# Optimization experiments

Hardware: AMD Instinct MI355X
Metric: run time of the kernel (lower is better)

Reference implementation:

```python
import jax, jax.numpy as jnp
import numpy as np

NEG_SLOPE = 0.2

def gat_conv(x, src, dst, W, a_src, a_dst, b, num_nodes, concat):
    # PyG GATConv (add_self_loops already applied to src/dst).
    H, C = a_src.shape
    h = (x @ W).reshape(-1, H, C)                      # [N,H,C]
    s = jnp.einsum('nhc,hc->nh', h, a_src)             # per-node src score
    d = jnp.einsum('nhc,hc->nh', h, a_dst)             # per-node dst score
    e = jax.nn.leaky_relu(s[src] + d[dst], NEG_SLOPE)  # [E,H]
    emax = jax.lax.stop_gradient(
        jax.ops.segment_max(e, dst, num_segments=num_nodes))  # [N,H]
    ex = jnp.exp(e - emax[dst])
    denom = jax.ops.segment_sum(ex, dst, num_segments=num_nodes)
    alpha = ex / denom[dst]                            # segment softmax over in-edges
    msg = h[src] * alpha[:, :, None]                   # [E,H,C]
    out = jax.ops.segment_sum(msg, dst, num_segments=num_nodes)
    out = out.reshape(num_nodes, H * C) if concat else out.mean(axis=1)
    return out + b

def setup_inputs() -> dict:
    key = jax.random.key(0)
    ks = jax.random.split(key, 20)
    N, E, F = 50000, 400000, 256
    x = jax.random.normal(ks[0], (N, F), dtype=jnp.float32)
    edge_index = jax.random.randint(ks[1], (2, E), 0, N, dtype=jnp.int64)
    def p(k, shape):
        return (jax.random.normal(k, shape, dtype=jnp.float32) * 0.1)
    inp = {'x': x, 'edge_index': edge_index}
    # conv1: 256 -> 8x32 ; conv2: 256 -> 4x32 ; conv3: 128 -> 2x32 ; conv4: 64 -> 1x32
    dims = [(256, 8, 32), (256, 4, 32), (128, 2, 32), (64, 1, 32)]
    ki = 2
    for i, (fin, H, C) in enumerate(dims, start=1):
        inp[f'W{i}'] = p(ks[ki], (fin, H * C)); ki += 1
        inp[f'a_src{i}'] = p(ks[ki], (H, C)); ki += 1
        inp[f'a_dst{i}'] = p(ks[ki], (H, C)); ki += 1
        bdim = H * C if i < 4 else C
        inp[f'b{i}'] = jnp.zeros((bdim,), dtype=jnp.float32)
    return inp

def reference(x, edge_index, W1, a_src1, a_dst1, b1, W2, a_src2, a_dst2, b2,
              W3, a_src3, a_dst3, b3, W4, a_src4, a_dst4, b4):
    N = x.shape[0]
    loops = jnp.arange(N, dtype=edge_index.dtype)
    src = jnp.concatenate([edge_index[0], loops])
    dst = jnp.concatenate([edge_index[1], loops])
    h = jax.nn.elu(gat_conv(x, src, dst, W1, a_src1, a_dst1, b1, N, True))
    h = jax.nn.elu(gat_conv(h, src, dst, W2, a_src2, a_dst2, b2, N, True))
    h = gat_conv(h, src, dst, W3, a_src3, a_dst3, b3, N, True)
    h = jax.nn.elu(h)
    h = gat_conv(h, src, dst, W4, a_src4, a_dst4, b4, N, False)
    return jax.nn.log_softmax(h, axis=1)
```

## Files before the change

kernel.cpp:

```cpp
#include <hip/hip_runtime.h>
#include <hip/hip_bf16.h>

#define LRELU_SLOPE 0.2f

typedef __attribute__((ext_vector_type(8))) short short8;
typedef __attribute__((ext_vector_type(4))) float f32x4;

__device__ __forceinline__ unsigned short bf16r(float f) {
    unsigned int u = __builtin_bit_cast(unsigned int, f);
    u += 0x7fffu + ((u >> 16) & 1u);
    return (unsigned short)(u >> 16);
}
__device__ __forceinline__ float bf2f(unsigned short u) {
    return __builtin_bit_cast(float, (unsigned int)u << 16);
}


#define WTOT 108544

__global__ void k_pre(const float* __restrict__ Wa, const float* __restrict__ Wb,
                      const float* __restrict__ Wc, const float* __restrict__ Wd,
                      unsigned short* __restrict__ Ta, unsigned short* __restrict__ Tb,
                      unsigned short* __restrict__ Tc, unsigned short* __restrict__ Td,
                      const int* __restrict__ ei, int* __restrict__ cnt, int E, int N) {
    int gid = blockIdx.x * blockDim.x + threadIdx.x;
    if (gid < WTOT) {
        int id = gid;
        const float* W; unsigned short* T; int K, Nc;
        if (id < 65536)       { W = Wa; T = Ta; K = 256; Nc = 256; }
        else if (id < 98304)  { id -= 65536;  W = Wb; T = Tb; K = 256; Nc = 128; }
        else if (id < 106496) { id -= 98304;  W = Wc; T = Tc; K = 128; Nc = 64; }
        else                  { id -= 106496; W = Wd; T = Td; K = 64;  Nc = 32; }
        int n = id / K, k = id % K;
        T[id] = bf16r(W[(long)k * Nc + n]);
        return;
    }
    int e = gid - WTOT;
    if (e >= E + N) return;
    int dst = (e < E) ? ei[E + e] : (e - E);
    atomicAdd(&cnt[dst], 1);
}


__global__ void k_scan_blk(const int* __restrict__ cnt, int* __restrict__ offs,
                           int* __restrict__ bsum, int N) {
    __shared__ int temp[1024];
    int t = threadIdx.x;
    int gi = blockIdx.x * 1024 + t;
    int v = (gi < N) ? cnt[gi] : 0;
    temp[t] = v;
    __syncthreads();
    for (int o = 1; o < 1024; o <<= 1) {
        int x = (t >= o) ? temp[t - o] : 0;
        __syncthreads();
        temp[t] += x;
        __syncthreads();
    }
    if (gi < N) offs[gi] = temp[t] - v;
    if (t == 1023) bsum[blockIdx.x] = temp[1023];
}

__global__ void k_scan(const int* __restrict__ cnt, int* __restrict__ offs, int N) {
    __shared__ int temp[1024];
    __shared__ int carry_s;
    int t = threadIdx.x;
    if (t == 0) carry_s = 0;
    __syncthreads();
    for (int base = 0; base < N; base += 1024) {
        int v = (base + t < N) ? cnt[base + t] : 0;
        temp[t] = v;
        __syncthreads();
        for (int o = 1; o < 1024; o <<= 1) {
            int x = (t >= o) ? temp[t - o] : 0;
            __syncthreads();
            temp[t] += x;
            __syncthreads();
        }
        int incl = temp[t];
        int carry = carry_s;
        if (base + t < N) offs[base + t] = carry + incl - v;
        __syncthreads();
        if (t == 1023) carry_s = carry + temp[1023];
        __syncthreads();
    }
    if (t == 0) offs[N] = carry_s;
}

__global__ void k_scan_add(int* __restrict__ offs, const int* __restrict__ bpre,
                           int* __restrict__ wp, int N, int nb) {
    int gi = blockIdx.x * blockDim.x + threadIdx.x;
    if (gi < N) {
        int v = offs[gi] + bpre[gi >> 10];
        offs[gi] = v;
        wp[gi] = v;
    } else if (gi == N) {
        offs[N] = bpre[nb];
    }
}

__global__ void k_scatter(const int* __restrict__ ei, int* __restrict__ wp,
                          int* __restrict__ adj, int E, int N) {
    int e = blockIdx.x * blockDim.x + threadIdx.x;
    if (e >= E + N) return;
    int srcn = (e < E) ? ei[e] : (e - E);
    int dst  = (e < E) ? ei[E + e] : (e - E);
    int pos = atomicAdd(&wp[dst], 1);
    adj[pos] = srcn;
}


#define PSTR 40

template<int BN, bool F32A>
__global__ __launch_bounds__(256) void k_mgemm(const void* __restrict__ Ain,
                                               const unsigned short* __restrict__ WT,
                                               unsigned short* __restrict__ Cb,
                                               const float* __restrict__ a_src,
                                               const float* __restrict__ a_dst,
                                               float* __restrict__ sbuf,
                                               float* __restrict__ dbuf,
                                               int M, int Nc, int K, int H) {
    constexpr int NBF = BN / 16;
    constexpr int BCH = BN / 64;
    constexpr int SP  = BN + 8;
    constexpr int CPR = BN / 32;
    __shared__ __align__(16) unsigned short LB[128 * PSTR + BN * PSTR];
    unsigned short* As = LB;
    unsigned short* Bs = LB + 128 * PSTR;

    int t = threadIdx.x;
    int wv = t >> 6, l = t & 63;
    int bm = blockIdx.y * 128, bn = blockIdx.x * BN;

    f32x4 acc[2][NBF];
#pragma unroll
    for (int i = 0; i < 2; ++i)
#pragma unroll
        for (int j = 0; j < NBF; ++j) acc[i][j] = (f32x4){0.f, 0.f, 0.f, 0.f};

    int ar0 = t >> 2, akc = t & 3;
    int ar1 = ar0 + 64;
    int grA0 = min(bm + ar0, M - 1);
    int grA1 = min(bm + ar1, M - 1);
    int bc[BCH], gcB[BCH];
#pragma unroll
    for (int i = 0; i < BCH; ++i) {
        bc[i] = (t >> 2) + i * 64;
        gcB[i] = min(bn + bc[i], Nc - 1);
    }

    int row_in = l & 15, quad = l >> 4;
    const short8* apf0 = (const short8*)&As[(wv * 32 + row_in) * PSTR + quad * 8];
    const short8* apf1 = (const short8*)&As[(wv * 32 + 16 + row_in) * PSTR + quad * 8];
    const short8* bpf[NBF];
#pragma unroll
    for (int f = 0; f < NBF; ++f)
        bpf[f] = (const short8*)&Bs[(f * 16 + row_in) * PSTR + quad * 8];

    for (int k0 = 0; k0 < K; k0 += 32) {
        if constexpr (F32A) {
            const float* Af = (const float*)Ain;
            {
                const float4* p = (const float4*)&Af[(long)grA0 * K + k0 + akc * 8];
                float4 f0 = p[0], f1 = p[1];
                short8 sv;
                sv[0] = (short)bf16r(f0.x); sv[1] = (short)bf16r(f0.y);
                sv[2] = (short)bf16r(f0.z); sv[3] = (short)bf16r(f0.w);
                sv[4] = (short)bf16r(f1.x); sv[5] = (short)bf16r(f1.y);
                sv[6] = (short)bf16r(f1.z); sv[7] = (short)bf16r(f1.w);
                *(short8*)&As[ar0 * PSTR + akc * 8] = sv;
            }
            {
                const float4* p = (const float4*)&Af[(long)grA1 * K + k0 + akc * 8];
                float4 f0 = p[0], f1 = p[1];
                short8 sv;
                sv[0] = (short)bf16r(f0.x); sv[1] = (short)bf16r(f0.y);
                sv[2] = (short)bf16r(f0.z); sv[3] = (short)bf16r(f0.w);
                sv[4] = (short)bf16r(f1.x); sv[5] = (short)bf16r(f1.y);
                sv[6] = (short)bf16r(f1.z); sv[7] = (short)bf16r(f1.w);
                *(short8*)&As[ar1 * PSTR + akc * 8] = sv;
            }
        } else {
            const unsigned short* Ab = (const unsigned short*)Ain;
            *(short8*)&As[ar0 * PSTR + akc * 8] =
                *(const short8*)&Ab[(long)grA0 * K + k0 + akc * 8];
            *(short8*)&As[ar1 * PSTR + akc * 8] =
                *(const short8*)&Ab[(long)grA1 * K + k0 + akc * 8];
        }
#pragma unroll
        for (int i = 0; i < BCH; ++i)
            *(short8*)&Bs[bc[i] * PSTR + akc * 8] =
                *(const short8*)&WT[(long)gcB[i] * K + k0 + akc * 8];
        __syncthreads();

        short8 a0 = *apf0, a1 = *apf1;
#pragma unroll
        for (int f = 0; f < NBF; ++f) {
            short8 b = *bpf[f];
            acc[0][f] = __builtin_amdgcn_mfma_f32_16x16x32_bf16(a0, b, acc[0][f], 0, 0, 0);
            acc[1][f] = __builtin_amdgcn_mfma_f32_16x16x32_bf16(a1, b, acc[1][f], 0, 0, 0);
        }
        __syncthreads();
    }

    int rr = t / CPR;
    int cc = t % CPR;
#pragma unroll
    for (int rt = 0; rt < 2; ++rt) {
#pragma unroll
        for (int r = 0; r < 4; ++r)
#pragma unroll
            for (int ct = 0; ct < NBF; ++ct)
                LB[(wv * 16 + quad * 4 + r) * SP + ct * 16 + row_in] =
                    bf16r(acc[rt][ct][r]);
        __syncthreads();
        if (rr < 64) {
            int grow = bm + ((rr >> 4) << 5) + rt * 16 + (rr & 15);
            int colb = bn + cc * 32;
            if (grow < M && colb < Nc) {
                const unsigned short* ep = &LB[rr * SP + cc * 32];
                short8 v0 = *(const short8*)(ep);
                short8 v1 = *(const short8*)(ep + 8);
                short8 v2 = *(const short8*)(ep + 16);
                short8 v3 = *(const short8*)(ep + 24);
                unsigned short* cp = &Cb[(long)grow * Nc + colb];
                *(short8*)(cp)      = v0;
                *(short8*)(cp + 8)  = v1;
                *(short8*)(cp + 16) = v2;
                *(short8*)(cp + 24) = v3;
                int hd = colb >> 5;
                const float* ap = a_src + hd * 32;
                const float* dp = a_dst + hd * 32;
                float ss = 0.f, dd = 0.f;
#pragma unroll
                for (int u = 0; u < 8; ++u) {
                    float va = bf2f((unsigned short)v0[u]); ss += va * ap[u];      dd += va * dp[u];
                    float vb = bf2f((unsigned short)v1[u]); ss += vb * ap[8 + u];  dd += vb * dp[8 + u];
                    float vc = bf2f((unsigned short)v2[u]); ss += vc * ap[16 + u]; dd += vc * dp[16 + u];
                    float vd = bf2f((unsigned short)v3[u]); ss += vd * ap[24 + u]; dd += vd * dp[24 + u];
                }
                sbuf[(long)grow * H + hd] = ss;
                dbuf[(long)grow * H + hd] = dd;
            }
        }
        __syncthreads();
    }
}


template<int ACT>
__global__ void k_aggf(const unsigned short* __restrict__ h, const float* __restrict__ s,
                       const float* __restrict__ dsc, const int* __restrict__ offs,
                       const int* __restrict__ adj, const float* __restrict__ bias,
                       unsigned short* __restrict__ out16, float* __restrict__ out32,
                       int N, int H) {
    const int C8 = 4;
    long tid = (long)blockIdx.x * blockDim.x + threadIdx.x;
    int HC8 = H * C8;
    if (tid >= (long)N * HC8) return;
    int c8 = (int)(tid % C8);
    int hh = (int)((tid / C8) % H);
    int n  = (int)(tid / HC8);
    int beg = offs[n], end = offs[n + 1];
    float dn = dsc[n * H + hh];
    int HC = HC8 * 8;
    int coff = hh * 32 + c8 * 8;

    float denom = 0.f;
    float acc[8];
#pragma unroll
    for (int u = 0; u < 8; ++u) acc[u] = 0.f;

    for (int j = beg; j < end; ++j) {
        int sn = adj[j];
        float e = s[sn * H + hh] + dn;
        e = e > 0.f ? e : LRELU_SLOPE * e;
        float w = __expf(fminf(e, 80.f));
        short8 hv = *(const short8*)(h + (size_t)sn * HC + coff);
        denom += w;
#pragma unroll
        for (int u = 0; u < 8; ++u)
            acc[u] += w * bf2f((unsigned short)hv[u]);
    }

    float inv = 1.0f / denom;
    float o[8];
#pragma unroll
    for (int u = 0; u < 8; ++u) o[u] = acc[u] * inv + bias[coff + u];

    if (ACT == 1) {
        short8 pk;
#pragma unroll
        for (int u = 0; u < 8; ++u) {
            float v = o[u] > 0.f ? o[u] : (__expf(o[u]) - 1.f);
            pk[u] = (short)bf16r(v);
        }
        *(short8*)(out16 + tid * 8) = pk;
    } else {
        float m = o[0];
#pragma unroll
        for (int u = 1; u < 8; ++u) m = fmaxf(m, o[u]);
        m = fmaxf(m, __shfl_xor(m, 1));
        m = fmaxf(m, __shfl_xor(m, 2));
        float ssum = 0.f;
#pragma unroll
        for (int u = 0; u < 8; ++u) ssum += __expf(o[u] - m);
        ssum += __shfl_xor(ssum, 1);
        ssum += __shfl_xor(ssum, 2);
        float lse = m + __logf(ssum);
        float4 lo = {o[0] - lse, o[1] - lse, o[2] - lse, o[3] - lse};
        float4 hi = {o[4] - lse, o[5] - lse, o[6] - lse, o[7] - lse};
        *(float4*)(out32 + tid * 8)     = lo;
        *(float4*)(out32 + tid * 8 + 4) = hi;
    }
}


static inline size_t align_up(size_t x) { return (x + 255) & ~(size_t)255; }

extern "C" void kernel_launch(void* const* d_in, const int* in_sizes, int n_in,
                              void* d_out, int out_size, void* d_ws, size_t ws_size,
                              hipStream_t stream) {
    const float* x   = (const float*)d_in[0];
    const int*   ei  = (const int*)d_in[1];

    const int N = in_sizes[0] / 256;
    const int E = in_sizes[1] / 2;
    const int ET = E + N;
    const int NB = (N + 1023) / 1024;

    size_t off = 0;
    char* ws = (char*)d_ws;
    auto take = [&](size_t bytes) { char* p = ws + off; off += align_up(bytes); return p; };
    int*   offs  = (int*)take((size_t)(N + 1) * 4);
    int*   wp    = (int*)take((size_t)N * 4);
    int*   adj   = (int*)take((size_t)ET * 4);
    int*   bsum  = (int*)take((size_t)(NB + 1) * 4);
    int*   bpre  = (int*)take((size_t)(NB + 1) * 4);
    float* sbuf  = (float*)take((size_t)N * 8 * 4);
    float* dbuf  = (float*)take((size_t)N * 8 * 4);
    unsigned short* Xb = (unsigned short*)take((size_t)N * 256 * 2);
    unsigned short* Yb = (unsigned short*)take((size_t)N * 256 * 2);
    unsigned short* WT0 = (unsigned short*)take((size_t)256 * 256 * 2);
    unsigned short* WT1 = (unsigned short*)take((size_t)256 * 128 * 2);
    unsigned short* WT2 = (unsigned short*)take((size_t)128 * 64 * 2);
    unsigned short* WT3 = (unsigned short*)take((size_t)64 * 32 * 2);
    (void)ws_size;

    hipMemsetAsync(wp, 0, (size_t)N * 4, stream);
    {
        long tot = WTOT + ET;
        k_pre<<<(int)((tot + 255) / 256), 256, 0, stream>>>(
            (const float*)d_in[2], (const float*)d_in[6], (const float*)d_in[10],
            (const float*)d_in[14], WT0, WT1, WT2, WT3, ei, wp, E, N);
        k_scan_blk<<<NB, 1024, 0, stream>>>(wp, offs, bsum, N);
        k_scan<<<1, 1024, 0, stream>>>(bsum, bpre, NB);
        k_scan_add<<<(N + 256) / 256, 256, 0, stream>>>(offs, bpre, wp, N, NB);
        k_scatter<<<(ET + 255) / 256, 256, 0, stream>>>(ei, wp, adj, E, N);
    }

    struct Layer { const float* as; const float* ad; const float* b;
                   const unsigned short* WT; int Fin; int H; };
    Layer layers[4] = {
        {(const float*)d_in[3],  (const float*)d_in[4],  (const float*)d_in[5],  WT0, 256, 8},
        {(const float*)d_in[7],  (const float*)d_in[8],  (const float*)d_in[9],  WT1, 256, 4},
        {(const float*)d_in[11], (const float*)d_in[12], (const float*)d_in[13], WT2, 128, 2},
        {(const float*)d_in[15], (const float*)d_in[16], (const float*)d_in[17], WT3,  64, 1},
    };

    for (int li = 0; li < 4; ++li) {
        Layer& L = layers[li];
        int HC = L.H * 32;
        int K = L.Fin;

        if (li == 0) {
            dim3 grd((HC + 127) / 128, (N + 127) / 128);
            k_mgemm<128, true><<<grd, 256, 0, stream>>>(x, L.WT, Yb, L.as, L.ad,
                                                        sbuf, dbuf, N, HC, K, L.H);
        } else if (HC >= 128) {
            dim3 grd(HC / 128, (N + 127) / 128);
            k_mgemm<128, false><<<grd, 256, 0, stream>>>(Xb, L.WT, Yb, L.as, L.ad,
                                                         sbuf, dbuf, N, HC, K, L.H);
        } else {
            dim3 grd((HC + 63) / 64, (N + 127) / 128);
            k_mgemm<64, false><<<grd, 256, 0, stream>>>(Xb, L.WT, Yb, L.as, L.ad,
                                                        sbuf, dbuf, N, HC, K, L.H);
        }
        {
            long total = (long)N * L.H * 4;
            int nb = (int)((total + 255) / 256);
            if (li < 3)
                k_aggf<1><<<nb, 256, 0, stream>>>(Yb, sbuf, dbuf, offs, adj, L.b,
                                                  Xb, nullptr, N, L.H);
            else
                k_aggf<0><<<nb, 256, 0, stream>>>(Yb, sbuf, dbuf, offs, adj, L.b,
                                                  nullptr, (float*)d_out, N, L.H);
        }
    }
}
```

Baseline: 349.2 us.

## Halve GEMM M-tile to 64 rows and prefetch next K-slice into registers

The projection GEMM now uses 64-row tiles instead of 128, doubling the grid and shrinking LDS and accumulator use, which should raise occupancy and spread work across more CUs. It also software-pipelines the K loop: global loads for the next 32-wide K slice are issued into registers while MFMAs run on the current slice. The epilogue collapses to a single pass. In exchange, W tiles are reloaded twice as often and each wave does half the MFMA work per LDS sync.

```diff
diff --git a/kernel.cpp b/kernel.cpp
--- a/kernel.cpp
+++ b/kernel.cpp
@@ -124,24 +124,23 @@
     constexpr int BCH = BN / 64;
     constexpr int SP  = BN + 8;
     constexpr int CPR = BN / 32;
-    __shared__ __align__(16) unsigned short LB[128 * PSTR + BN * PSTR];
+    constexpr int STAGE = 64 * PSTR + BN * PSTR;
+    constexpr int EPIL  = 64 * SP;
+    constexpr int LBSZ  = STAGE > EPIL ? STAGE : EPIL;
+    __shared__ __align__(16) unsigned short LB[LBSZ];
     unsigned short* As = LB;
-    unsigned short* Bs = LB + 128 * PSTR;
+    unsigned short* Bs = LB + 64 * PSTR;
 
     int t = threadIdx.x;
     int wv = t >> 6, l = t & 63;
-    int bm = blockIdx.y * 128, bn = blockIdx.x * BN;
-
-    f32x4 acc[2][NBF];
-#pragma unroll
-    for (int i = 0; i < 2; ++i)
-#pragma unroll
-        for (int j = 0; j < NBF; ++j) acc[i][j] = (f32x4){0.f, 0.f, 0.f, 0.f};
-
-    int ar0 = t >> 2, akc = t & 3;
-    int ar1 = ar0 + 64;
-    int grA0 = min(bm + ar0, M - 1);
-    int grA1 = min(bm + ar1, M - 1);
+    int bm = blockIdx.y * 64, bn = blockIdx.x * BN;
+
+    f32x4 acc[NBF];
+#pragma unroll
+    for (int j = 0; j < NBF; ++j) acc[j] = (f32x4){0.f, 0.f, 0.f, 0.f};
+
+    int ar = t >> 2, akc = t & 3;
+    int grA = min(bm + ar, M - 1);
     int bc[BCH], gcB[BCH];
 #pragma unroll
     for (int i = 0; i < BCH; ++i) {
@@ -150,100 +149,107 @@
     }
 
     int row_in = l & 15, quad = l >> 4;
-    const short8* apf0 = (const short8*)&As[(wv * 32 + row_in) * PSTR + quad * 8];
-    const short8* apf1 = (const short8*)&As[(wv * 32 + 16 + row_in) * PSTR + quad * 8];
+    const short8* apf = (const short8*)&As[(wv * 16 + row_in) * PSTR + quad * 8];
     const short8* bpf[NBF];
 #pragma unroll
     for (int f = 0; f < NBF; ++f)
         bpf[f] = (const short8*)&Bs[(f * 16 + row_in) * PSTR + quad * 8];
 
+    const float* Af = (const float*)Ain;
+    const unsigned short* Ab = (const unsigned short*)Ain;
+
+    float4 af0, af1, af0n, af1n;
+    short8 ab8, ab8n;
+    short8 bb[BCH], bbn[BCH];
+
+    if constexpr (F32A) {
+        const float4* p = (const float4*)&Af[(long)grA * K + akc * 8];
+        af0 = p[0]; af1 = p[1];
+    } else {
+        ab8 = *(const short8*)&Ab[(long)grA * K + akc * 8];
+    }
+#pragma unroll
+    for (int i = 0; i < BCH; ++i)
+        bb[i] = *(const short8*)&WT[(long)gcB[i] * K + akc * 8];
+
     for (int k0 = 0; k0 < K; k0 += 32) {
+        short8 av;
         if constexpr (F32A) {
-            const float* Af = (const float*)Ain;
-            {
-                const float4* p = (const float4*)&Af[(long)grA0 * K + k0 + akc * 8];
-                float4 f0 = p[0], f1 = p[1];
-                short8 sv;
-                sv[0] = (short)bf16r(f0.x); sv[1] = (short)bf16r(f0.y);
-                sv[2] = (short)bf16r(f0.z); sv[3] = (short)bf16r(f0.w);
-                sv[4] = (short)bf16r(f1.x); sv[5] = (short)bf16r(f1.y);
-                sv[6] = (short)bf16r(f1.z); sv[7] = (short)bf16r(f1.w);
-                *(short8*)&As[ar0 * PSTR + akc * 8] = sv;
+            av[0] = (short)bf16r(af0.x); av[1] = (short)bf16r(af0.y);
+            av[2] = (short)bf16r(af0.z); av[3] = (short)bf16r(af0.w);
+            av[4] = (short)bf16r(af1.x); av[5] = (short)bf16r(af1.y);
+            av[6] = (short)bf16r(af1.z); av[7] = (short)bf16r(af1.w);
+        } else {
+            av = ab8;
+        }
+        *(short8*)&As[ar * PSTR + akc * 8] = av;
+#pragma unroll
+        for (int i = 0; i < BCH; ++i)
+            *(short8*)&Bs[bc[i] * PSTR + akc * 8] = bb[i];
+        __syncthreads();
+
+        int kn = k0 + 32;
+        if (kn < K) {
+            if constexpr (F32A) {
+                const float4* p = (const float4*)&Af[(long)grA * K + kn + akc * 8];
+                af0n = p[0]; af1n = p[1];
+            } else {
+                ab8n = *(const short8*)&Ab[(long)grA * K + kn + akc * 8];
             }
-            {
-                const float4* p = (const float4*)&Af[(long)grA1 * K + k0 + akc * 8];
-                float4 f0 = p[0], f1 = p[1];
-                short8 sv;
-                sv[0] = (short)bf16r(f0.x); sv[1] = (short)bf16r(f0.y);
-                sv[2] = (short)bf16r(f0.z); sv[3] = (short)bf16r(f0.w);
-                sv[4] = (short)bf16r(f1.x); sv[5] = (short)bf16r(f1.y);
-                sv[6] = (short)bf16r(f1.z); sv[7] = (short)bf16r(f1.w);
-                *(short8*)&As[ar1 * PSTR + akc * 8] = sv;
-            }
-        } else {
-            const unsigned short* Ab = (const unsigned short*)Ain;
-            *(short8*)&As[ar0 * PSTR + akc * 8] =
-                *(const short8*)&Ab[(long)grA0 * K + k0 + akc * 8];
-            *(short8*)&As[ar1 * PSTR + akc * 8] =
-                *(const short8*)&Ab[(long)grA1 * K + k0 + akc * 8];
-        }
-#pragma unroll
-        for (int i = 0; i < BCH; ++i)
-            *(short8*)&Bs[bc[i] * PSTR + akc * 8] =
-                *(const short8*)&WT[(long)gcB[i] * K + k0 + akc * 8];
-        __syncthreads();
-
-        short8 a0 = *apf0, a1 = *apf1;
+#pragma unroll
+            for (int i = 0; i < BCH; ++i)
+                bbn[i] = *(const short8*)&WT[(long)gcB[i] * K + kn + akc * 8];
+        }
+
+        short8 a0 = *apf;
 #pragma unroll
         for (int f = 0; f < NBF; ++f) {
             short8 b = *bpf[f];
-            acc[0][f] = __builtin_amdgcn_mfma_f32_16x16x32_bf16(a0, b, acc[0][f], 0, 0, 0);
-            acc[1][f] = __builtin_amdgcn_mfma_f32_16x16x32_bf16(a1, b, acc[1][f], 0, 0, 0);
-        }
-        __syncthreads();
-    }
-
-    int rr = t / CPR;
-    int cc = t % CPR;
-#pragma unroll
-    for (int rt = 0; rt < 2; ++rt) {
-#pragma unroll
-        for (int r = 0; r < 4; ++r)
-#pragma unroll
-            for (int ct = 0; ct < NBF; ++ct)
-                LB[(wv * 16 + quad * 4 + r) * SP + ct * 16 + row_in] =
-                    bf16r(acc[rt][ct][r]);
-        __syncthreads();
-        if (rr < 64) {
-            int grow = bm + ((rr >> 4) << 5) + rt * 16 + (rr & 15);
-            int colb = bn + cc * 32;
-            if (grow < M && colb < Nc) {
-                const unsigned short* ep = &LB[rr * SP + cc * 32];
-                short8 v0 = *(const short8*)(ep);
-                short8 v1 = *(const short8*)(ep + 8);
-                short8 v2 = *(const short8*)(ep + 16);
-                short8 v3 = *(const short8*)(ep + 24);
-                unsigned short* cp = &Cb[(long)grow * Nc + colb];
-                *(short8*)(cp)      = v0;
-                *(short8*)(cp + 8)  = v1;
-                *(short8*)(cp + 16) = v2;
-                *(short8*)(cp + 24) = v3;
-                int hd = colb >> 5;
-                const float* ap = a_src + hd * 32;
-                const float* dp = a_dst + hd * 32;
-                float ss = 0.f, dd = 0.f;
-#pragma unroll
-                for (int u = 0; u < 8; ++u) {
-                    float va = bf2f((unsigned short)v0[u]); ss += va * ap[u];      dd += va * dp[u];
-                    float vb = bf2f((unsigned short)v1[u]); ss += vb * ap[8 + u];  dd += vb * dp[8 + u];
-                    float vc = bf2f((unsigned short)v2[u]); ss += vc * ap[16 + u]; dd += vc * dp[16 + u];
-                    float vd = bf2f((unsigned short)v3[u]); ss += vd * ap[24 + u]; dd += vd * dp[24 + u];
-                }
-                sbuf[(long)grow * H + hd] = ss;
-                dbuf[(long)grow * H + hd] = dd;
+            acc[f] = __builtin_amdgcn_mfma_f32_16x16x32_bf16(a0, b, acc[f], 0, 0, 0);
+        }
+        __syncthreads();
+
+        af0 = af0n; af1 = af1n; ab8 = ab8n;
+#pragma unroll
+        for (int i = 0; i < BCH; ++i) bb[i] = bbn[i];
+    }
+
+#pragma unroll
+    for (int r = 0; r < 4; ++r)
+#pragma unroll
+        for (int ct = 0; ct < NBF; ++ct)
+            LB[(wv * 16 + quad * 4 + r) * SP + ct * 16 + row_in] = bf16r(acc[ct][r]);
+    __syncthreads();
+
+    int rr = t / CPR, cc = t % CPR;
+    if (rr < 64) {
+        int grow = bm + rr;
+        int colb = bn + cc * 32;
+        if (grow < M && colb < Nc) {
+            const unsigned short* ep = &LB[rr * SP + cc * 32];
+            short8 v0 = *(const short8*)(ep);
+            short8 v1 = *(const short8*)(ep + 8);
+            short8 v2 = *(const short8*)(ep + 16);
+            short8 v3 = *(const short8*)(ep + 24);
+            unsigned short* cp = &Cb[(long)grow * Nc + colb];
+            *(short8*)(cp)      = v0;
+            *(short8*)(cp + 8)  = v1;
+            *(short8*)(cp + 16) = v2;
+            *(short8*)(cp + 24) = v3;
+            int hd = colb >> 5;
+            const float* ap = a_src + hd * 32;
+            const float* dp = a_dst + hd * 32;
+            float ss = 0.f, dd = 0.f;
+#pragma unroll
+            for (int u = 0; u < 8; ++u) {
+                float va = bf2f((unsigned short)v0[u]); ss += va * ap[u];      dd += va * dp[u];
+                float vb = bf2f((unsigned short)v1[u]); ss += vb * ap[8 + u];  dd += vb * dp[8 + u];
+                float vc = bf2f((unsigned short)v2[u]); ss += vc * ap[16 + u]; dd += vc * dp[16 + u];
+                float vd = bf2f((unsigned short)v3[u]); ss += vd * ap[24 + u]; dd += vd * dp[24 + u];
             }
-        }
-        __syncthreads();
+            sbuf[(long)grow * H + hd] = ss;
+            dbuf[(long)grow * H + hd] = dd;
+        }
     }
 }
 
@@ -374,15 +380,15 @@
         int K = L.Fin;
 
         if (li == 0) {
-            dim3 grd((HC + 127) / 128, (N + 127) / 128);
+            dim3 grd((HC + 127) / 128, (N + 63) / 64);
             k_mgemm<128, true><<<grd, 256, 0, stream>>>(x, L.WT, Yb, L.as, L.ad,
                                                         sbuf, dbuf, N, HC, K, L.H);
         } else if (HC >= 128) {
-            dim3 grd(HC / 128, (N + 127) / 128);
+            dim3 grd(HC / 128, (N + 63) / 64);
             k_mgemm<128, false><<<grd, 256, 0, stream>>>(Xb, L.WT, Yb, L.as, L.ad,
                                                          sbuf, dbuf, N, HC, K, L.H);
         } else {
-            dim3 grd((HC + 63) / 64, (N + 127) / 128);
+            dim3 grd((HC + 63) / 64, (N + 63) / 64);
             k_mgemm<64, false><<<grd, 256, 0, stream>>>(Xb, L.WT, Yb, L.as, L.ad,
                                                         sbuf, dbuf, N, HC, K, L.H);
         }
```

Result: no change. 349.4 us (+0.0%).
